# Optimization experiments

Measured on AMD Instinct MI355X. Metric: run time of the kernel, lower is better.

Reference implementation:

```python
import jax, jax.numpy as jnp
import numpy as np

LN_EPS = 1e-5

def _layernorm(x, g, b):
    m = jnp.mean(x, axis=-1, keepdims=True)
    v = jnp.var(x, axis=-1, keepdims=True)
    return (x - m) * jax.lax.rsqrt(v + LN_EPS) * g + b

def setup_inputs() -> dict:
    key = jax.random.key(0)
    ks = jax.random.split(key, 8)
    H = 1024
    B, S = 8, 2048
    def xavier(k, fan_in, fan_out):
        lim = float(np.sqrt(6.0 / (fan_in + fan_out)))
        return jax.random.uniform(k, (fan_in, fan_out), jnp.float32, -lim, lim)
    return {
        "x": jax.random.normal(ks[0], (B, S, H), jnp.float32),
        "hidden_state": jnp.zeros((B, H), jnp.float32),
        "W_in": xavier(ks[1], H, 3 * H), "b_in": jnp.zeros((3 * H,), jnp.float32),
        "W_rec": xavier(ks[2], H, H), "b_rec": jnp.zeros((H,), jnp.float32),
        "W_gate": xavier(ks[3], H, 2 * H), "b_gate": jnp.zeros((2 * H,), jnp.float32),
        "W_out": xavier(ks[4], H, H), "b_out": jnp.zeros((H,), jnp.float32),
        "ln_g": jnp.ones((H,), jnp.float32), "ln_b": jnp.zeros((H,), jnp.float32),
    }

def reference(x, hidden_state, W_in, b_in, W_rec, b_rec, W_gate, b_gate, W_out, b_out, ln_g, ln_b):
    # x: [B, S, H]
    H = x.shape[-1]
    feats = jnp.einsum('bsh,hk->bsk', x, W_in) + b_in        # [B,S,3H]
    u, v, w = jnp.split(feats, 3, axis=-1)
    u = jax.nn.silu(u)
    v = jax.nn.silu(v)
    # scan over time: xs laid out [S, B, H]
    uvw = (u.swapaxes(0, 1), v.swapaxes(0, 1), w.swapaxes(0, 1))

    def step(h, xs_t):
        u_t, v_t, w_t = xs_t
        gf = h @ W_gate + b_gate                              # [B,2H]
        gv, gt = jnp.split(gf, 2, axis=-1)
        gate = jax.nn.sigmoid(gv) * jax.nn.silu(gt)
        rec = h @ W_rec + b_rec
        nh = gate * rec + (1.0 - gate) * (u_t * v_t + w_t)
        nh = _layernorm(nh, ln_g, ln_b)                       # dropout inactive (eval)
        return nh, nh

    final_hidden, hiddens = jax.lax.scan(step, hidden_state, uvw)  # hiddens: [S,B,H]
    output = jnp.einsum('sbh,hk->bsk', hiddens, W_out) + b_out     # [B,S,H]
    return output, final_hidden
```

## Files before the change

kernel.cpp:

```cpp
#include <hip/hip_runtime.h>
#include <stdint.h>
#include <stddef.h>

typedef _Float16 f16;
typedef __attribute__((ext_vector_type(8))) _Float16 f16x8;
typedef __attribute__((ext_vector_type(4))) _Float16 f16x4;
typedef __attribute__((ext_vector_type(4))) float     f32x4;
typedef __attribute__((ext_vector_type(2))) float     f32x2;
typedef unsigned long long u64;

#define NB 8
#define NS 2048
#define NHID 1024
#define NWG 64

__device__ __forceinline__ float fsig(float x)  { return 1.f/(1.f+__expf(-x)); }
__device__ __forceinline__ float fsilu(float x) { return x/(1.f+__expf(-x)); }

__global__ __launch_bounds__(256) void k_cvt_f16(const float* __restrict__ in,
                                                 f16* __restrict__ out, int n) {
  int i = (blockIdx.x*blockDim.x + threadIdx.x)*4;
  int stride = gridDim.x*blockDim.x*4;
  for (; i < n; i += stride) {
    f32x4 v = *(const f32x4*)(in + i);
    f16x4 o = { (f16)v[0], (f16)v[1], (f16)v[2], (f16)v[3] };
    *(f16x4*)(out + i) = o;
  }
}

__global__ __launch_bounds__(256) void k_transpose_cvt(const float* __restrict__ W,
                                                       f16* __restrict__ Wt,
                                                       int K, int N) {
  __shared__ float tile[32][33];
  int k0 = blockIdx.x*32, n0 = blockIdx.y*32;
  int tx = threadIdx.x & 31, ty = threadIdx.x >> 5;
  for (int i = ty; i < 32; i += 8) tile[i][tx] = W[(size_t)(k0+i)*N + n0 + tx];
  __syncthreads();
  for (int i = ty; i < 32; i += 8) Wt[(size_t)(n0+i)*K + k0 + tx] = (f16)tile[tx][i];
}

__global__ __launch_bounds__(256) void k_gemm1(const f16* __restrict__ A,
                                               const f16* __restrict__ Bt,
                                               const float* __restrict__ b_in,
                                               f16* __restrict__ z) {
  __shared__ f16 As[2][128*64];
  __shared__ f16 Bs[2][3][32*64];
  const int tid  = threadIdx.x;
  const int row0 = blockIdx.x * 128;
  const int j0   = blockIdx.y * 32;
  const int lane = tid & 63, wave = tid >> 6;
  const int wm = wave >> 1, wj = wave & 1;

  f32x4 acc[4][3];
  const f32x4 zv = {0.f,0.f,0.f,0.f};
#pragma unroll
  for (int m = 0; m < 4; ++m)
#pragma unroll
    for (int s = 0; s < 3; ++s) acc[m][s] = zv;

  f16x8 ar[4]; f16x8 br[3];

  auto loadT = [&](int kt) {
    int k0 = kt*64;
#pragma unroll
    for (int i = 0; i < 4; ++i) {
      int c = tid + i*256; int r = c >> 3;
      ar[i] = *(const f16x8*)(A + (size_t)(row0 + r)*1024 + k0 + (c & 7)*8);
    }
#pragma unroll
    for (int i = 0; i < 3; ++i) {
      int c = tid + i*256; int strip = c >> 8; int cc = c & 255; int r = cc >> 3;
      br[i] = *(const f16x8*)(Bt + (size_t)(strip*1024 + j0 + r)*1024 + k0 + (cc & 7)*8);
    }
  };
  auto writeT = [&](int buf) {
#pragma unroll
    for (int i = 0; i < 4; ++i) {
      int c = tid + i*256; int r = c >> 3; int kb = (c & 7)*16;
      *(f16x8*)((char*)As[buf] + r*128 + (kb ^ ((r & 7) << 4))) = ar[i];
    }
#pragma unroll
    for (int i = 0; i < 3; ++i) {
      int c = tid + i*256; int strip = c >> 8; int cc = c & 255; int r = cc >> 3; int kb = (cc & 7)*16;
      *(f16x8*)((char*)Bs[buf][strip] + r*128 + (kb ^ ((r & 7) << 4))) = br[i];
    }
  };
  auto compute = [&](int buf) {
    const char* Ab = (const char*)As[buf];
#pragma unroll
    for (int kk = 0; kk < 2; ++kk) {
      int kq = kk*64 + ((lane >> 4) << 4);
      f16x8 af[4];
#pragma unroll
      for (int mt = 0; mt < 4; ++mt) {
        int r = wm*64 + mt*16 + (lane & 15);
        af[mt] = *(const f16x8*)(Ab + r*128 + (kq ^ ((r & 7) << 4)));
      }
#pragma unroll
      for (int st = 0; st < 3; ++st) {
        int cB = wj*16 + (lane & 15);
        f16x8 bf = *(const f16x8*)((const char*)Bs[buf][st] + cB*128 + (kq ^ ((cB & 7) << 4)));
#pragma unroll
        for (int mt = 0; mt < 4; ++mt)
          acc[mt][st] = __builtin_amdgcn_mfma_f32_16x16x32_f16(af[mt], bf, acc[mt][st], 0, 0, 0);
      }
    }
  };

  loadT(0); writeT(0);
  __syncthreads();
  for (int kt = 0; kt < 16; ++kt) {
    int cur = kt & 1;
    if (kt + 1 < 16) loadT(kt+1);
    compute(cur);
    if (kt + 1 < 16) writeT(cur ^ 1);
    __syncthreads();
  }

  const int jc = j0 + wj*16 + (lane & 15);
  const float bu = b_in[jc], bv = b_in[1024 + jc], bw = b_in[2048 + jc];
#pragma unroll
  for (int mt = 0; mt < 4; ++mt) {
#pragma unroll
    for (int i = 0; i < 4; ++i) {
      int r = row0 + wm*64 + mt*16 + ((lane >> 4) << 2) + i;
      float u = acc[mt][0][i] + bu;
      float v = acc[mt][1][i] + bv;
      float w = acc[mt][2][i] + bw;
      float zz = fsilu(u)*fsilu(v) + w;
      int b_ = r >> 11, s_ = r & 2047;
      z[(((size_t)s_*64 + (jc >> 4))*8 + b_)*16 + (jc & 15)] = (f16)zz;
    }
  }
}

__global__ __launch_bounds__(256) void k_gemm3(const f16* __restrict__ A,
                                               const f16* __restrict__ Bt,
                                               const float* __restrict__ b_out,
                                               float* __restrict__ out) {
  __shared__ f16 As[2][128*64];
  __shared__ f16 Bs[2][32*64];
  const int tid  = threadIdx.x;
  const int row0 = blockIdx.x * 128;
  const int n0   = blockIdx.y * 32;
  const int lane = tid & 63, wave = tid >> 6;
  const int wm = wave >> 1, wn = wave & 1;

  f32x4 acc[4];
  const f32x4 zv = {0.f,0.f,0.f,0.f};
#pragma unroll
  for (int m = 0; m < 4; ++m) acc[m] = zv;

  f16x8 ar[4]; f16x8 br1;

  auto loadT = [&](int kt) {
    int k0 = kt*64;
#pragma unroll
    for (int i = 0; i < 4; ++i) {
      int c = tid + i*256; int r = c >> 3;
      ar[i] = *(const f16x8*)(A + (size_t)(row0 + r)*1024 + k0 + (c & 7)*8);
    }
    { int c = tid; int r = c >> 3;
      br1 = *(const f16x8*)(Bt + (size_t)(n0 + r)*1024 + k0 + (c & 7)*8); }
  };
  auto writeT = [&](int buf) {
#pragma unroll
    for (int i = 0; i < 4; ++i) {
      int c = tid + i*256; int r = c >> 3; int kb = (c & 7)*16;
      *(f16x8*)((char*)As[buf] + r*128 + (kb ^ ((r & 7) << 4))) = ar[i];
    }
    { int c = tid; int r = c >> 3; int kb = (c & 7)*16;
      *(f16x8*)((char*)Bs[buf] + r*128 + (kb ^ ((r & 7) << 4))) = br1; }
  };
  auto compute = [&](int buf) {
    const char* Ab = (const char*)As[buf];
#pragma unroll
    for (int kk = 0; kk < 2; ++kk) {
      int kq = kk*64 + ((lane >> 4) << 4);
      int cB = wn*16 + (lane & 15);
      f16x8 bf = *(const f16x8*)((const char*)Bs[buf] + cB*128 + (kq ^ ((cB & 7) << 4)));
#pragma unroll
      for (int mt = 0; mt < 4; ++mt) {
        int r = wm*64 + mt*16 + (lane & 15);
        f16x8 af = *(const f16x8*)(Ab + r*128 + (kq ^ ((r & 7) << 4)));
        acc[mt] = __builtin_amdgcn_mfma_f32_16x16x32_f16(af, bf, acc[mt], 0, 0, 0);
      }
    }
  };

  loadT(0); writeT(0);
  __syncthreads();
  for (int kt = 0; kt < 16; ++kt) {
    int cur = kt & 1;
    if (kt + 1 < 16) loadT(kt+1);
    compute(cur);
    if (kt + 1 < 16) writeT(cur ^ 1);
    __syncthreads();
  }

  const int n = n0 + wn*16 + (lane & 15);
  const float bo = b_out[n];
#pragma unroll
  for (int mt = 0; mt < 4; ++mt) {
#pragma unroll
    for (int i = 0; i < 4; ++i) {
      int r = row0 + wm*64 + mt*16 + ((lane >> 4) << 2) + i;
      int s = r >> 3, b = r & 7;
      out[(size_t)b*(NS*NHID) + (size_t)s*NHID + n] = acc[mt][i] + bo;
    }
  }
}

#define SCAN_LDS 54208
__global__ __launch_bounds__(256, 1) void k_scan(
    const float* __restrict__ h0g,  const float* __restrict__ Wg,
    const float* __restrict__ bg,   const float* __restrict__ Wr,
    const float* __restrict__ brv,  const float* __restrict__ lng_g,
    const float* __restrict__ lnb_g,const f16* __restrict__ z,
    f16* __restrict__ hid,          u64* __restrict__ hpub,
    float* __restrict__ finalh) {
  extern __shared__ char smem[];
  f16*   hlds = (f16*)smem;
  float* redw = (float*)(smem + 33536);
  f32x2* gb   = (f32x2*)(smem + 45824);
  float* bia  = (float*)(smem + 54016);

  const int tid  = threadIdx.x;
  const int wg   = blockIdx.x;
  const int wave = tid >> 6, lane = tid & 63;
  const int r8   = tid >> 5, g32 = tid & 31;
  const int rr   = (tid >> 4) & 7, cc = tid & 15;
  const int rL   = tid & 7;
  const int c2L  = (tid & 63) >> 3;

  f16x8 wf0[8], wf1[8], wf2[8];
  {
    const int cB = wg*16 + (lane & 15);
    const int kq = (lane >> 4) << 3;
#pragma unroll
    for (int ks = 0; ks < 8; ++ks) {
      int k = wave*256 + ks*32 + kq;
      f16x8 a, b, c;
#pragma unroll
      for (int e = 0; e < 8; ++e) {
        a[e] = (f16)Wg[(size_t)(k+e)*2048 + cB];
        b[e] = (f16)Wg[(size_t)(k+e)*2048 + 1024 + cB];
        c[e] = (f16)Wr[(size_t)(k+e)*1024 + cB];
      }
      wf0[ks] = a; wf1[ks] = b; wf2[ks] = c;
    }
  }
  for (int i = tid; i < 1024; i += 256) { f32x2 p = { lng_g[i], lnb_g[i] }; gb[i] = p; }
  if (tid < 48)
    bia[tid] = (tid < 16) ? bg[wg*16 + tid]
             : (tid < 32) ? bg[1024 + wg*16 + (tid-16)]
                          : brv[wg*16 + (tid-32)];
  for (int i = tid; i < 8*1048; i += 256) hlds[8*1048 + i] = (f16)0.f;
  __syncthreads();

  for (int t = 0; t <= NS; ++t) {
    f16 zreg = (f16)0.f;
    if (t < NS && tid < 128) zreg = z[(((size_t)t*64 + wg)*8 + rr)*16 + cc];

    if (t == 0) {
#pragma unroll
      for (int j = 0; j < 8; ++j) {
        f32x4 v = *(const f32x4*)(h0g + r8*1024 + (j*32 + g32)*4);
        int colb = j*128 + g32*4;
        f16x4 hv = { (f16)v[0], (f16)v[1], (f16)v[2], (f16)v[3] };
        *(f16x4*)(hlds + r8*1048 + colb) = hv;
      }
      __syncthreads();
    } else {
      const u64* src = hpub + (size_t)(t & 1)*4096;
      u64 got[16];
      for (;;) {
        unsigned ok = 1;
#pragma unroll
        for (int i = 0; i < 16; ++i) {
          got[i] = __hip_atomic_load(src + i*256 + tid,
                                     __ATOMIC_RELAXED, __HIP_MEMORY_SCOPE_AGENT);
          ok &= (unsigned)((unsigned)(got[i] >> 32) == (unsigned)t);
        }
        if (ok) break;
      }
      float vals[32];
      float sum = 0.f, sq = 0.f;
#pragma unroll
      for (int i = 0; i < 16; ++i) {
        unsigned lo = (unsigned)got[i];
        float va = (float)__builtin_bit_cast(f16, (unsigned short)(lo & 0xffff));
        float vb = (float)__builtin_bit_cast(f16, (unsigned short)(lo >> 16));
        vals[2*i] = va; vals[2*i+1] = vb;
        sum += va + vb; sq += va*va + vb*vb;
      }
#pragma unroll
      for (int off = 8; off <= 32; off <<= 1) {
        sum += __shfl_xor(sum, off, 64);
        sq  += __shfl_xor(sq,  off, 64);
      }
      if (lane < 8) { f32x2 p = { sum, sq }; ((f32x2*)redw)[wave*8 + lane] = p; }
      __syncthreads();
      float s4 = 0.f, q4 = 0.f;
#pragma unroll
      for (int w2 = 0; w2 < 4; ++w2) {
        f32x2 p = ((const f32x2*)redw)[w2*8 + rL];
        s4 += p[0]; q4 += p[1];
      }
      float m  = s4 * (1.f/1024.f);
      float va = q4 * (1.f/1024.f) - m*m;
      float rs = rsqrtf(va + 1e-5f);
#pragma unroll
      for (int i = 0; i < 16; ++i) {
        int wgI = i*4 + wave;
        int col = wgI*16 + c2L*2;
        f32x4 gg = *(const f32x4*)(gb + col);
        float h0n = (vals[2*i]   - m)*rs*gg[0] + gg[1];
        float h1n = (vals[2*i+1] - m)*rs*gg[2] + gg[3];
        unsigned w32 = (unsigned)__builtin_bit_cast(unsigned short, (f16)h0n)
                     | ((unsigned)__builtin_bit_cast(unsigned short, (f16)h1n) << 16);
        *(unsigned*)((char*)hlds + rL*2096 + col*2) = w32;
      }
      __syncthreads();
    }

    if (t >= 1 && tid < 32) {
      int row = tid >> 2, ch = tid & 3;
      u64 v = *(const u64*)(hlds + row*1048 + wg*16 + ch*4);
      *(u64*)(hid + ((size_t)(t-1)*8 + row)*1024 + wg*16 + ch*4) = v;
    }
    if (t == NS) {
      if (tid < 128) finalh[rr*1024 + wg*16 + cc] = (float)hlds[rr*1048 + wg*16 + cc];
      break;
    }

    f32x4 acc0 = {0,0,0,0}, acc1 = {0,0,0,0}, acc2 = {0,0,0,0};
    {
      const char* hb = (const char*)hlds + (lane & 15)*2096;
      const int kbyte0 = (wave*256 + ((lane >> 4) << 3))*2;
#pragma unroll
      for (int ks = 0; ks < 8; ++ks) {
        f16x8 af = *(const f16x8*)(hb + kbyte0 + ks*64);
        acc0 = __builtin_amdgcn_mfma_f32_16x16x32_f16(af, wf0[ks], acc0, 0, 0, 0);
        acc1 = __builtin_amdgcn_mfma_f32_16x16x32_f16(af, wf1[ks], acc1, 0, 0, 0);
        acc2 = __builtin_amdgcn_mfma_f32_16x16x32_f16(af, wf2[ks], acc2, 0, 0, 0);
      }
    }
    *(f32x4*)(redw + ((wave*3 + 0)*64 + lane)*4) = acc0;
    *(f32x4*)(redw + ((wave*3 + 1)*64 + lane)*4) = acc1;
    *(f32x4*)(redw + ((wave*3 + 2)*64 + lane)*4) = acc2;
    __syncthreads();

    if (tid < 128) {
      int li  = ((rr >> 2) << 4) + cc;
      int reg = rr & 3;
      float s0 = 0.f, s1 = 0.f, s2 = 0.f;
#pragma unroll
      for (int q = 0; q < 4; ++q) {
        s0 += redw[((q*3 + 0)*64 + li)*4 + reg];
        s1 += redw[((q*3 + 1)*64 + li)*4 + reg];
        s2 += redw[((q*3 + 2)*64 + li)*4 + reg];
      }
      float gv = s0 + bia[cc];
      float gt = s1 + bia[16 + cc];
      float rc = s2 + bia[32 + cc];
      float gate = fsig(gv) * fsilu(gt);
      float nh   = gate*rc + (1.f - gate)*(float)zreg;
      float nh_hi = __shfl_xor(nh, 1, 64);
      if ((cc & 1) == 0) {
        u64 v = (u64)__builtin_bit_cast(unsigned short, (f16)nh)
              | ((u64)__builtin_bit_cast(unsigned short, (f16)nh_hi) << 16)
              | ((u64)(unsigned)(t + 1) << 32);
        __hip_atomic_store(hpub + (size_t)((t + 1) & 1)*4096 + wg*64 + (cc >> 1)*8 + rr,
                           v, __ATOMIC_RELAXED, __HIP_MEMORY_SCOPE_AGENT);
      }
    }
  }
}

extern "C" void kernel_launch(void* const* d_in, const int* in_sizes, int n_in,
                              void* d_out, int out_size, void* d_ws, size_t ws_size,
                              hipStream_t stream) {
  const float* x      = (const float*)d_in[0];
  const float* h0     = (const float*)d_in[1];
  const float* W_in   = (const float*)d_in[2];
  const float* b_in   = (const float*)d_in[3];
  const float* W_rec  = (const float*)d_in[4];
  const float* b_rec  = (const float*)d_in[5];
  const float* W_gate = (const float*)d_in[6];
  const float* b_gate = (const float*)d_in[7];
  const float* W_out  = (const float*)d_in[8];
  const float* b_out  = (const float*)d_in[9];
  const float* ln_g   = (const float*)d_in[10];
  const float* ln_b   = (const float*)d_in[11];
  float* out = (float*)d_out;

  char* ws = (char*)d_ws;
  f16*   x_f16  = (f16*)(ws);
  f16*   Wt_in  = (f16*)(ws + 33554432);
  f16*   Wt_out = (f16*)(ws + 39845888);
  f16*   z      = (f16*)(ws + 41943040);
  f16*   hid    = (f16*)(ws + 75497472);
  u64*   hpub   = (u64*)(ws + 109051904);

  k_cvt_f16<<<2048, 256, 0, stream>>>(x, x_f16, NB*NS*NHID);
  { dim3 g(32, 96); k_transpose_cvt<<<g, 256, 0, stream>>>(W_in,  Wt_in,  1024, 3072); }
  { dim3 g(32, 32); k_transpose_cvt<<<g, 256, 0, stream>>>(W_out, Wt_out, 1024, 1024); }

  { dim3 g(128, 32); k_gemm1<<<g, 256, 0, stream>>>(x_f16, Wt_in, b_in, z); }

  hipFuncSetAttribute((const void*)k_scan, hipFuncAttributeMaxDynamicSharedMemorySize, SCAN_LDS);
  k_scan<<<NWG, 256, SCAN_LDS, stream>>>(h0, W_gate, b_gate, W_rec, b_rec,
                                         ln_g, ln_b, z, hid, hpub,
                                         out + (size_t)NB*NS*NHID);

  { dim3 g(128, 32); k_gemm3<<<g, 256, 0, stream>>>(hid, Wt_out, b_out, out); }
}
```

Measured before the change: 7.113 ms.

## Replace tagged per-element polling with per-workgroup flags and release/acquire fences

The cross-workgroup handoff of the hidden state in the scan kernel changes. Before, every thread polled sixteen 64-bit words that each carried a step tag. Now each workgroup writes plain 32-bit f16 pairs, issues a release fence and a barrier, then bumps a single per-workgroup tag. Consumers spin on the 64 tags with one wave, acquire, and then load the payload normally. This cuts polling traffic and payload size, but adds an extra barrier, fences and a second dependent memory round-trip on every step of the latency-bound serial loop.

```diff
diff --git a/kernel.cpp b/kernel.cpp
--- a/kernel.cpp
+++ b/kernel.cpp
@@ -8,6 +8,7 @@
 typedef __attribute__((ext_vector_type(4))) float     f32x4;
 typedef __attribute__((ext_vector_type(2))) float     f32x2;
 typedef unsigned long long u64;
+typedef unsigned int u32;
 
 #define NB 8
 #define NS 2048
@@ -217,8 +218,8 @@
     const float* __restrict__ bg,   const float* __restrict__ Wr,
     const float* __restrict__ brv,  const float* __restrict__ lng_g,
     const float* __restrict__ lnb_g,const f16* __restrict__ z,
-    f16* __restrict__ hid,          u64* __restrict__ hpub,
-    float* __restrict__ finalh) {
+    f16* __restrict__ hid,          u32* __restrict__ hpay,
+    u32* __restrict__ tags,         float* __restrict__ finalh) {
   extern __shared__ char smem[];
   f16*   hlds = (f16*)smem;
   float* redw = (float*)(smem + 33536);
@@ -272,23 +273,24 @@
       }
       __syncthreads();
     } else {
-      const u64* src = hpub + (size_t)(t & 1)*4096;
-      u64 got[16];
-      for (;;) {
-        unsigned ok = 1;
-#pragma unroll
-        for (int i = 0; i < 16; ++i) {
-          got[i] = __hip_atomic_load(src + i*256 + tid,
-                                     __ATOMIC_RELAXED, __HIP_MEMORY_SCOPE_AGENT);
-          ok &= (unsigned)((unsigned)(got[i] >> 32) == (unsigned)t);
-        }
-        if (ok) break;
-      }
+      if (tid < 64) {
+        while (__hip_atomic_load(&tags[tid], __ATOMIC_RELAXED,
+                                 __HIP_MEMORY_SCOPE_AGENT) < (u32)t) { }
+        __builtin_amdgcn_fence(__ATOMIC_ACQUIRE, "agent");
+      }
+      __syncthreads();
+
+      const u32* __restrict__ src = hpay + (size_t)(t & 1)*4096;
+      u32 got[16];
+#pragma unroll
+      for (int i = 0; i < 16; ++i)
+        got[i] = src[rL*512 + 32*i + 8*wave + c2L];
+
       float vals[32];
       float sum = 0.f, sq = 0.f;
 #pragma unroll
       for (int i = 0; i < 16; ++i) {
-        unsigned lo = (unsigned)got[i];
+        u32 lo = got[i];
         float va = (float)__builtin_bit_cast(f16, (unsigned short)(lo & 0xffff));
         float vb = (float)__builtin_bit_cast(f16, (unsigned short)(lo >> 16));
         vals[2*i] = va; vals[2*i+1] = vb;
@@ -317,9 +319,9 @@
         f32x4 gg = *(const f32x4*)(gb + col);
         float h0n = (vals[2*i]   - m)*rs*gg[0] + gg[1];
         float h1n = (vals[2*i+1] - m)*rs*gg[2] + gg[3];
-        unsigned w32 = (unsigned)__builtin_bit_cast(unsigned short, (f16)h0n)
-                     | ((unsigned)__builtin_bit_cast(unsigned short, (f16)h1n) << 16);
-        *(unsigned*)((char*)hlds + rL*2096 + col*2) = w32;
+        u32 w32 = (u32)__builtin_bit_cast(unsigned short, (f16)h0n)
+                | ((u32)__builtin_bit_cast(unsigned short, (f16)h1n) << 16);
+        *(u32*)((char*)hlds + rL*2096 + col*2) = w32;
       }
       __syncthreads();
     }
@@ -368,13 +370,16 @@
       float nh   = gate*rc + (1.f - gate)*(float)zreg;
       float nh_hi = __shfl_xor(nh, 1, 64);
       if ((cc & 1) == 0) {
-        u64 v = (u64)__builtin_bit_cast(unsigned short, (f16)nh)
-              | ((u64)__builtin_bit_cast(unsigned short, (f16)nh_hi) << 16)
-              | ((u64)(unsigned)(t + 1) << 32);
-        __hip_atomic_store(hpub + (size_t)((t + 1) & 1)*4096 + wg*64 + (cc >> 1)*8 + rr,
-                           v, __ATOMIC_RELAXED, __HIP_MEMORY_SCOPE_AGENT);
-      }
-    }
+        u32 v = (u32)__builtin_bit_cast(unsigned short, (f16)nh)
+              | ((u32)__builtin_bit_cast(unsigned short, (f16)nh_hi) << 16);
+        hpay[(size_t)((t + 1) & 1)*4096 + rr*512 + wg*8 + (cc >> 1)] = v;
+      }
+      __builtin_amdgcn_fence(__ATOMIC_RELEASE, "agent");
+    }
+    __syncthreads();
+    if (tid == 0)
+      __hip_atomic_store(&tags[wg], (u32)(t + 1),
+                         __ATOMIC_RELAXED, __HIP_MEMORY_SCOPE_AGENT);
   }
 }
 
@@ -401,7 +406,10 @@
   f16*   Wt_out = (f16*)(ws + 39845888);
   f16*   z      = (f16*)(ws + 41943040);
   f16*   hid    = (f16*)(ws + 75497472);
-  u64*   hpub   = (u64*)(ws + 109051904);
+  u32*   hpay   = (u32*)(ws + 109051904);
+  u32*   tags   = (u32*)(ws + 109084672);
+
+  (void)hipMemsetAsync(tags, 0, 256, stream);
 
   k_cvt_f16<<<2048, 256, 0, stream>>>(x, x_f16, NB*NS*NHID);
   { dim3 g(32, 96); k_transpose_cvt<<<g, 256, 0, stream>>>(W_in,  Wt_in,  1024, 3072); }
@@ -409,9 +417,9 @@
 
   { dim3 g(128, 32); k_gemm1<<<g, 256, 0, stream>>>(x_f16, Wt_in, b_in, z); }
 
-  hipFuncSetAttribute((const void*)k_scan, hipFuncAttributeMaxDynamicSharedMemorySize, SCAN_LDS);
+  (void)hipFuncSetAttribute((const void*)k_scan, hipFuncAttributeMaxDynamicSharedMemorySize, SCAN_LDS);
   k_scan<<<NWG, 256, SCAN_LDS, stream>>>(h0, W_gate, b_gate, W_rec, b_rec,
-                                         ln_g, ln_b, z, hid, hpub,
+                                         ln_g, ln_b, z, hid, hpay, tags,
                                          out + (size_t)NB*NS*NHID);
 
   { dim3 g(128, 32); k_gemm3<<<g, 256, 0, stream>>>(hid, Wt_out, b_out, out); }
```

New measurement: 14.32 ms. +101.4%, slower.
